# Kernel optimization log

Measured on AMD Instinct MI355X. Metric: run time of the kernel, lower is better.

## Reference

```python
import jax, jax.numpy as jnp
import numpy as np

B, S, H = 2, 256, 512
EPS = 1e-12  # TPLinker conditional LayerNorm default epsilon
NEG = -1e30  # finite stand-in for -inf in running max


def _cond_layer_norm(x, cond, Wg, Wb, gamma, beta):
    # TPLinker conditional LayerNorm: gamma/beta are modulated by a linear map of cond.
    g = gamma + cond @ Wg          # (..., H)
    b = beta + cond @ Wb           # (..., H)
    xc = x - jnp.mean(x, axis=-1, keepdims=True)
    inv = jax.lax.rsqrt(jnp.mean(xc * xc, axis=-1, keepdims=True) + EPS)
    return xc * inv * g + b


def setup_inputs() -> dict:
    key = jax.random.key(0)
    ks = jax.random.split(key, 6)
    return {
        "seq_hiddens": jax.random.normal(ks[0], (B, S, H), jnp.float32),
        "mask": jnp.ones((B, S), jnp.float32),
        "lamtha": jax.random.uniform(ks[1], (H,), jnp.float32),
        "Wg1": jax.random.normal(ks[2], (H, H), jnp.float32) * 0.02,
        "Wb1": jax.random.normal(ks[3], (H, H), jnp.float32) * 0.02,
        "g1": jnp.ones((H,), jnp.float32),
        "b1": jnp.zeros((H,), jnp.float32),
        "Wg2": jax.random.normal(ks[4], (H, H), jnp.float32) * 0.02,
        "Wb2": jax.random.normal(ks[5], (H, H), jnp.float32) * 0.02,
        "g2": jnp.ones((H,), jnp.float32),
        "b2": jnp.zeros((H,), jnp.float32),
    }


def reference(seq_hiddens, mask, lamtha, Wg1, Wb1, g1, b1, Wg2, Wb2, g2, b2):
    # mask additive penalty, broadcast over hidden (matches (1-mask)*-1000 expand)
    seq = seq_hiddens + ((1.0 - mask) * -1000.0)[:, :, None]  # (B,S,H)

    ii, jj = jnp.triu_indices(S)  # row-major pairs (i, j>=i), same order as the torch loop

    # window means over seq[i..j] via cumulative sums (replaces O(S^3) recomputation)
    csum = jnp.cumsum(seq, axis=1)                              # (B,S,H)
    lens = (jj - ii + 1).astype(seq.dtype)[None, :, None]
    mean_pairs = (csum[:, jj] - csum[:, ii] + seq[:, ii]) / lens  # (B,P,H)

    # window maxes over seq[i..j]: scan over j keeping running max per start i
    idx = jnp.arange(S)

    def step(state, j):
        sj = jnp.take(seq, j, axis=1)  # (B,H)
        new = jnp.where((idx <= j)[None, :, None],
                        jnp.maximum(state, sj[:, None, :]),
                        jnp.asarray(NEG, seq.dtype))
        return new, new

    _, Mall = jax.lax.scan(step, jnp.full((B, S, H), NEG, seq.dtype), idx)  # (S_j,B,S_i,H)
    max_pairs = Mall[jj, :, ii].transpose(1, 0, 2)  # (B,P,H)

    # mix pooling
    inner = lamtha * mean_pairs + (1.0 - lamtha) * max_pairs  # (B,P,H)

    visible = seq[:, jj]  # (B,P,H) token j
    repeat = seq[:, ii]   # (B,P,H) token i

    shaking = _cond_layer_norm(visible, repeat, Wg1, Wb1, g1, b1)
    return _cond_layer_norm(shaking, inner, Wg2, Wb2, g2, b2)
```

## Files before the change

kernel.cpp:

```cpp
#include <hip/hip_runtime.h>
#include <hip/hip_bf16.h>

typedef __hip_bfloat16 bf16;
typedef short short8 __attribute__((ext_vector_type(8)));
typedef float floatx4 __attribute__((ext_vector_type(4)));

#define S 256
#define H 512
#define P 32896
#define NROWS 65792
#define NEGF -1e30f
#define EPSF 1e-12f

#define OFF_SEQ    0u
#define OFF_CSUM   1048576u
#define OFF_LN1    2129920u
#define OFF_G1     3178496u
#define OFF_B1     4227072u
#define OFF_WCAT   5275648u
#define OFF_II     6324224u
#define OFF_JJ     6390016u
#define OFF_MU2    6455808u
#define OFF_INV2   6718976u
#define OFF_INNER  6982144u

__device__ __forceinline__ void gld_lds16(const void* g, void* l) {
    __builtin_amdgcn_global_load_lds(
        (const __attribute__((address_space(1))) void*)g,
        (__attribute__((address_space(3))) void*)l, 16, 0, 0);
}

__global__ __launch_bounds__(512) void prep_kernel(const float* __restrict__ Wg2,
                                                   const float* __restrict__ Wb2,
                                                   bf16* __restrict__ wcatT,
                                                   unsigned short* __restrict__ ii,
                                                   unsigned short* __restrict__ jj) {
    if (blockIdx.x < 1024) {
        int n = blockIdx.x, k = threadIdx.x;
        int tt = n >> 7, c = n & 127;
        int h = tt * 64 + (c & 63);
        float v = (c < 64) ? Wg2[(size_t)k * H + h] : Wb2[(size_t)k * H + h];
        wcatT[(size_t)n * H + k] = __float2bfloat16(v);
    } else {
        int p = (blockIdx.x - 1024) * 512 + threadIdx.x;
        if (p >= P) return;
        float disc = 513.0f * 513.0f - 8.0f * (float)p;
        int i = (int)((513.0f - sqrtf(disc)) * 0.5f);
        i = i < 0 ? 0 : (i > S - 1 ? S - 1 : i);
        while (i > 0 && (i * S - i * (i - 1) / 2) > p) --i;
        while (i < S - 1 && ((i + 1) * S - (i + 1) * i / 2) <= p) ++i;
        int off = i * S - i * (i - 1) / 2;
        ii[p] = (unsigned short)i;
        jj[p] = (unsigned short)(i + (p - off));
    }
}

__global__ __launch_bounds__(512) void seq_scan1_ln1(const float* __restrict__ x,
                                                     const float* __restrict__ mask,
                                                     float* __restrict__ seq, float* __restrict__ tot,
                                                     float* __restrict__ ln1) {
    __shared__ float part[8][8][2];
    __shared__ float rstat[8][2];
    int b = blockIdx.x >> 5, sc = blockIdx.x & 31, h = threadIdx.x;
    int wave = h >> 6, lane = h & 63;
    int s0 = sc * 8;
    float v[8];
    float run = 0.0f;
#pragma unroll
    for (int t = 0; t < 8; ++t) {
        int s = s0 + t;
        v[t] = x[(size_t)(b * S + s) * H + h] + (1.0f - mask[b * S + s]) * (-1000.0f);
        seq[(size_t)(b * S + s) * H + h] = v[t];
        run += v[t];
    }
    tot[(size_t)blockIdx.x * H + h] = run;
#pragma unroll
    for (int t = 0; t < 8; ++t) {
        float s = v[t], q = v[t] * v[t];
        for (int o = 1; o < 64; o <<= 1) { s += __shfl_xor(s, o); q += __shfl_xor(q, o); }
        if (lane == 0) { part[wave][t][0] = s; part[wave][t][1] = q; }
    }
    __syncthreads();
    if (h < 16) {
        int row = h >> 1, st = h & 1;
        float a = 0.0f;
#pragma unroll
        for (int w = 0; w < 8; ++w) a += part[w][row][st];
        rstat[row][st] = a;
    }
    __syncthreads();
#pragma unroll
    for (int t = 0; t < 8; ++t) {
        float m = rstat[t][0] * (1.0f / 512.0f);
        float var = rstat[t][1] * (1.0f / 512.0f) - m * m;
        var = var < 0.0f ? 0.0f : var;
        float inv = rsqrtf(var + EPSF);
        ln1[(size_t)(b * S + s0 + t) * H + h] = (v[t] - m) * inv;
    }
}

__global__ __launch_bounds__(512) void seq_scan2(const float* __restrict__ seq,
                                                 const float* __restrict__ tot,
                                                 float* __restrict__ csum) {
    int b = blockIdx.x >> 5, sc = blockIdx.x & 31, h = threadIdx.x;
    float run = 0.0f;
    for (int c = 0; c < sc; ++c) run += tot[(size_t)(b * 32 + c) * H + h];
    int s0 = sc * 8;
#pragma unroll
    for (int t = 0; t < 8; ++t) {
        run += seq[(size_t)(b * S + s0 + t) * H + h];
        csum[(size_t)(b * S + s0 + t) * H + h] = run;
    }
}

__global__ __launch_bounds__(512) void g1b1_kernel(
    const float* __restrict__ seq, const float* __restrict__ Wg1, const float* __restrict__ Wb1,
    const float* __restrict__ g1, const float* __restrict__ b1,
    float* __restrict__ G1, float* __restrict__ B1) {
    __shared__ float rowbuf[4][H];
    int grp = blockIdx.x;
    int mat = blockIdx.y;
    int h = threadIdx.x;
    int r0 = grp * 4;
    for (int r = 0; r < 4; ++r) rowbuf[r][h] = seq[(size_t)(r0 + r) * H + h];
    __syncthreads();
    const float* W = mat ? Wb1 : Wg1;
    float acc[4] = {0, 0, 0, 0};
#pragma unroll 8
    for (int k = 0; k < H; ++k) {
        float w = W[(size_t)k * H + h];
#pragma unroll
        for (int r = 0; r < 4; ++r) acc[r] += rowbuf[r][k] * w;
    }
    float bias = (mat ? b1 : g1)[h];
    float* dst = mat ? B1 : G1;
    for (int r = 0; r < 4; ++r) dst[(size_t)(r0 + r) * H + h] = acc[r] + bias;
}

__global__ __launch_bounds__(256) void inner_kernel(
    const float* __restrict__ seq, const float* __restrict__ csum,
    const float* __restrict__ lamtha, bf16* __restrict__ inner) {
    int id = blockIdx.x;
    int t = id & 255, b = id >> 8;
    int i = b ? (255 - t) : t;
    int h2 = threadIdx.x;
    float2 lam = ((const float2*)lamtha)[h2];
    float2 oml = {1.0f - lam.x, 1.0f - lam.y};
    const float2* seqb = (const float2*)(seq + (size_t)b * S * H);
    const float2* csb = (const float2*)(csum + (size_t)b * S * H);
    float2 s_i = seqb[i * 256 + h2];
    float2 c_i = csb[i * 256 + h2];
    float2 mrun = {NEGF, NEGF};
    size_t base = (size_t)b * P + (size_t)(i * S - i * (i - 1) / 2);
    __hip_bfloat162* dst = (__hip_bfloat162*)inner;
    int j = i;
#define INNER_STEP(vv, cc, jx)                                             \
    {                                                                      \
        mrun.x = fmaxf(mrun.x, vv.x);                                      \
        mrun.y = fmaxf(mrun.y, vv.y);                                      \
        float rl = 1.0f / (float)((jx) - i + 1);                           \
        float mx = (cc.x - c_i.x + s_i.x) * rl;                            \
        float my = (cc.y - c_i.y + s_i.y) * rl;                            \
        __hip_bfloat162 o;                                                 \
        o.x = __float2bfloat16(lam.x * mx + oml.x * mrun.x);               \
        o.y = __float2bfloat16(lam.y * my + oml.y * mrun.y);               \
        dst[(base + (size_t)((jx) - i)) * 256 + h2] = o;                   \
    }
    for (; j + 4 <= S; j += 4) {
        float2 v0 = seqb[(j + 0) * 256 + h2], c0 = csb[(j + 0) * 256 + h2];
        float2 v1 = seqb[(j + 1) * 256 + h2], c1 = csb[(j + 1) * 256 + h2];
        float2 v2 = seqb[(j + 2) * 256 + h2], c2 = csb[(j + 2) * 256 + h2];
        float2 v3 = seqb[(j + 3) * 256 + h2], c3 = csb[(j + 3) * 256 + h2];
        INNER_STEP(v0, c0, j + 0)
        INNER_STEP(v1, c1, j + 1)
        INNER_STEP(v2, c2, j + 2)
        INNER_STEP(v3, c3, j + 3)
    }
    for (; j < S; ++j) {
        float2 v = seqb[j * 256 + h2];
        float2 c = csb[j * 256 + h2];
        INNER_STEP(v, c, j)
    }
#undef INNER_STEP
}

__global__ void stats_kernel(const float* __restrict__ ln1, const float* __restrict__ G1,
                             const float* __restrict__ B1,
                             const unsigned short* __restrict__ ii,
                             const unsigned short* __restrict__ jj,
                             float* __restrict__ mu2, float* __restrict__ inv2) {
    int r = blockIdx.x * 4 + (threadIdx.x >> 6);
    int lane = threadIdx.x & 63;
    int b = (r >= P) ? 1 : 0;
    int p = r - b * P;
    int i = ii[p], j = jj[p];
    const float4* lp = (const float4*)(ln1 + (size_t)(b * S + j) * H);
    const float4* gp = (const float4*)(G1 + (size_t)(b * S + i) * H);
    const float4* bp = (const float4*)(B1 + (size_t)(b * S + i) * H);
    float sum = 0.0f, ss = 0.0f;
#pragma unroll
    for (int t = 0; t < 2; ++t) {
        int idx = t * 64 + lane;
        float4 a = lp[idx], g = gp[idx], bb = bp[idx];
        float v0 = a.x * g.x + bb.x, v1 = a.y * g.y + bb.y;
        float v2 = a.z * g.z + bb.z, v3 = a.w * g.w + bb.w;
        sum += (v0 + v1) + (v2 + v3);
        ss += (v0 * v0 + v1 * v1) + (v2 * v2 + v3 * v3);
    }
    for (int o = 1; o < 64; o <<= 1) { sum += __shfl_xor(sum, o); ss += __shfl_xor(ss, o); }
    if (lane == 0) {
        float m = sum * (1.0f / 512.0f);
        float var = ss * (1.0f / 512.0f) - m * m;
        var = var < 0.0f ? 0.0f : var;
        mu2[r] = m;
        inv2[r] = rsqrtf(var + EPSF);
    }
}

__global__ __launch_bounds__(256, 2) void gemm_kernel(
    const bf16* __restrict__ inner, const bf16* __restrict__ wcatT,
    const float* __restrict__ g2, const float* __restrict__ b2,
    const float* __restrict__ ln1, const float* __restrict__ G1, const float* __restrict__ B1,
    const unsigned short* __restrict__ ii, const unsigned short* __restrict__ jj,
    const float* __restrict__ mu2, const float* __restrict__ inv2,
    float* __restrict__ out) {
    extern __shared__ __align__(16) char smem[];

    const int tid = threadIdx.x;
    const int wave = tid >> 6, lane = tid & 63;
    const int q = lane >> 4, l15 = lane & 15;
    const int wm = wave & 1, wn = wave >> 1;

    const int id = blockIdx.x;
    int rb, t;
    if (id < 4096) { rb = (id >> 6) * 8 + (id & 7); t = (id >> 3) & 7; }
    else           { int w = id - 4096; rb = 512 + (w & 1); t = w >> 1; }
    const int R0 = rb * 128;

    const int srow = tid >> 3;
    const int sx8 = ((tid & 7) ^ (srow & 7)) * 8;
    const bf16* const Ag = inner + (size_t)(R0 + srow) * H + sx8;
    const bf16* const Bg = wcatT + (size_t)(t * 128 + srow) * H + sx8;

    char* const A0 = smem;
    char* const B0 = smem + 16384;
    char* const A1 = smem + 32768;
    char* const B1s = smem + 49152;

    floatx4 acc[4][4];
#pragma unroll
    for (int a = 0; a < 4; ++a)
#pragma unroll
        for (int c = 0; c < 4; ++c) acc[a][c] = (floatx4){0.f, 0.f, 0.f, 0.f};

    auto STAGE = [&](int kt, char* Ad, char* Bd) {
#pragma unroll
        for (int i2 = 0; i2 < 4; ++i2)
            gld_lds16(Ag + (size_t)i2 * 32 * H + kt * 64, Ad + i2 * 4096 + wave * 1024);
#pragma unroll
        for (int i2 = 0; i2 < 4; ++i2)
            gld_lds16(Bg + (size_t)i2 * 32 * H + kt * 64, Bd + i2 * 4096 + wave * 1024);
    };

    STAGE(0, A0, B0);
    STAGE(1, A1, B1s);
    asm volatile("s_waitcnt vmcnt(8)" ::: "memory");
    asm volatile("s_barrier" ::: "memory");

#pragma unroll
    for (int kt = 0; kt < 8; ++kt) {
        char* const As = (kt & 1) ? A1 : A0;
        char* const Bs = (kt & 1) ? B1s : B0;

        short8 bfr[4][2], af[4][2];
#pragma unroll
        for (int ks = 0; ks < 2; ++ks) {
#pragma unroll
            for (int fn = 0; fn < 4; ++fn) {
                int nr = (fn < 2 ? wn * 32 + fn * 16 : 64 + wn * 32 + (fn - 2) * 16) + l15;
                bfr[fn][ks] = *(const short8*)(Bs + nr * 128 + (((ks * 4 + q) ^ (l15 & 7)) << 4));
            }
#pragma unroll
            for (int fm = 0; fm < 4; ++fm) {
                int mr = wm * 64 + fm * 16 + l15;
                af[fm][ks] = *(const short8*)(As + mr * 128 + (((ks * 4 + q) ^ (l15 & 7)) << 4));
            }
        }

        __builtin_amdgcn_s_setprio(1);
#pragma unroll
        for (int fm = 0; fm < 4; ++fm)
#pragma unroll
            for (int fn = 0; fn < 4; ++fn)
                acc[fm][fn] = __builtin_amdgcn_mfma_f32_16x16x32_bf16(af[fm][0], bfr[fn][0], acc[fm][fn], 0, 0, 0);
        __builtin_amdgcn_s_setprio(0);

        if (kt < 6) {
            asm volatile("s_waitcnt lgkmcnt(0)" ::: "memory");
            asm volatile("s_barrier" ::: "memory");
            STAGE(kt + 2, As, Bs);
        }

        __builtin_amdgcn_s_setprio(1);
#pragma unroll
        for (int fm = 0; fm < 4; ++fm)
#pragma unroll
            for (int fn = 0; fn < 4; ++fn)
                acc[fm][fn] = __builtin_amdgcn_mfma_f32_16x16x32_bf16(af[fm][1], bfr[fn][1], acc[fm][fn], 0, 0, 0);
        __builtin_amdgcn_s_setprio(0);

        if (kt < 6) {
            asm volatile("s_waitcnt vmcnt(8)" ::: "memory");
            asm volatile("s_barrier" ::: "memory");
        } else if (kt == 6) {
            asm volatile("s_waitcnt vmcnt(0)" ::: "memory");
            asm volatile("s_barrier" ::: "memory");
        }
    }

    float g2v[2], b2v[2];
#pragma unroll
    for (int fg = 0; fg < 2; ++fg) {
        int h = t * 64 + wn * 32 + fg * 16 + l15;
        g2v[fg] = g2[h];
        b2v[fg] = b2[h];
    }
#pragma unroll
    for (int fm = 0; fm < 4; ++fm) {
#pragma unroll
        for (int r = 0; r < 4; ++r) {
            int m = wm * 64 + fm * 16 + q * 4 + r;
            int rg = R0 + m;
            int b = (rg >= P) ? 1 : 0;
            int p = rg - b * P;
            int i = ii[p], j = jj[p];
            float mu = mu2[rg], iv = inv2[rg];
            const float* lp = ln1 + (size_t)(b * S + j) * H + t * 64 + wn * 32;
            const float* gp = G1 + (size_t)(b * S + i) * H + t * 64 + wn * 32;
            const float* bp = B1 + (size_t)(b * S + i) * H + t * 64 + wn * 32;
            float* op = out + (size_t)rg * H + t * 64 + wn * 32;
#pragma unroll
            for (int fg = 0; fg < 2; ++fg) {
                int c = fg * 16 + l15;
                float s = (lp[c] * gp[c] + bp[c] - mu) * iv;
                float G2v = acc[fm][fg][r] + g2v[fg];
                float B2v = acc[fm][fg + 2][r] + b2v[fg];
                op[c] = s * G2v + B2v;
            }
        }
    }
}

extern "C" void kernel_launch(void* const* d_in, const int* in_sizes, int n_in,
                              void* d_out, int out_size, void* d_ws, size_t ws_size,
                              hipStream_t stream) {
    const float* x = (const float*)d_in[0];
    const float* mask = (const float*)d_in[1];
    const float* lamtha = (const float*)d_in[2];
    const float* Wg1 = (const float*)d_in[3];
    const float* Wb1 = (const float*)d_in[4];
    const float* g1 = (const float*)d_in[5];
    const float* b1 = (const float*)d_in[6];
    const float* Wg2 = (const float*)d_in[7];
    const float* Wb2 = (const float*)d_in[8];
    const float* g2 = (const float*)d_in[9];
    const float* b2 = (const float*)d_in[10];
    float* out = (float*)d_out;

    char* ws = (char*)d_ws;
    float* seq = (float*)(ws + OFF_SEQ);
    float* csum = (float*)(ws + OFF_CSUM);
    float* ln1 = (float*)(ws + OFF_LN1);
    float* G1 = (float*)(ws + OFF_G1);
    float* B1 = (float*)(ws + OFF_B1);
    bf16* wcatT = (bf16*)(ws + OFF_WCAT);
    unsigned short* iiA = (unsigned short*)(ws + OFF_II);
    unsigned short* jjA = (unsigned short*)(ws + OFF_JJ);
    float* mu2 = (float*)(ws + OFF_MU2);
    float* inv2 = (float*)(ws + OFF_INV2);
    bf16* inner = (bf16*)(ws + OFF_INNER);
    float* tot = (float*)(ws + OFF_INNER);

    static bool attr_set = false;
    if (!attr_set) {
        hipFuncSetAttribute((const void*)gemm_kernel,
                            hipFuncAttributeMaxDynamicSharedMemorySize, 65536);
        attr_set = true;
    }

    hipLaunchKernelGGL(prep_kernel, dim3(1089), dim3(512), 0, stream, Wg2, Wb2, wcatT, iiA, jjA);
    hipLaunchKernelGGL(seq_scan1_ln1, dim3(64), dim3(512), 0, stream, x, mask, seq, tot, ln1);
    hipLaunchKernelGGL(seq_scan2, dim3(64), dim3(512), 0, stream, seq, tot, csum);
    hipLaunchKernelGGL(g1b1_kernel, dim3(128, 2), dim3(512), 0, stream, seq, Wg1, Wb1, g1, b1, G1, B1);
    hipLaunchKernelGGL(inner_kernel, dim3(512), dim3(256), 0, stream, seq, csum, lamtha, inner);
    hipLaunchKernelGGL(stats_kernel, dim3(16448), dim3(256), 0, stream, ln1, G1, B1, iiA, jjA, mu2, inv2);
    hipLaunchKernelGGL(gemm_kernel, dim3(4112), dim3(256), 65536, stream,
                       inner, wcatT, g2, b2, ln1, G1, B1, iiA, jjA, mu2, inv2, out);
}
```

Baseline: 313.4 us.

## Fuse prep kernels and fold LN2 row stats into the inner pooling kernel

Merges the prep and first-scan kernels into one launch, and the second scan and G1/B1 matvec into another, cutting the launch count from seven to four. The per-pair LayerNorm-2 statistics are now computed inside the inner pooling kernel, which already walks every (i,j) pair, so the separate stats kernel that reread ln1/G1/B1 per pair goes away. The G1/B1 matvec also reads LDS rows as float4. In exchange the inner kernel does extra wave shuffles and LDS writes per j, which lengthens its serial loop, and there are only 512 blocks to carry that work.

```diff
diff --git a/kernel.cpp b/kernel.cpp
--- a/kernel.cpp
+++ b/kernel.cpp
@@ -30,131 +30,148 @@
         (__attribute__((address_space(3))) void*)l, 16, 0, 0);
 }
 
-__global__ __launch_bounds__(512) void prep_kernel(const float* __restrict__ Wg2,
-                                                   const float* __restrict__ Wb2,
-                                                   bf16* __restrict__ wcatT,
-                                                   unsigned short* __restrict__ ii,
-                                                   unsigned short* __restrict__ jj) {
-    if (blockIdx.x < 1024) {
-        int n = blockIdx.x, k = threadIdx.x;
-        int tt = n >> 7, c = n & 127;
-        int h = tt * 64 + (c & 63);
-        float v = (c < 64) ? Wg2[(size_t)k * H + h] : Wb2[(size_t)k * H + h];
-        wcatT[(size_t)n * H + k] = __float2bfloat16(v);
-    } else {
-        int p = (blockIdx.x - 1024) * 512 + threadIdx.x;
-        if (p >= P) return;
-        float disc = 513.0f * 513.0f - 8.0f * (float)p;
-        int i = (int)((513.0f - sqrtf(disc)) * 0.5f);
-        i = i < 0 ? 0 : (i > S - 1 ? S - 1 : i);
-        while (i > 0 && (i * S - i * (i - 1) / 2) > p) --i;
-        while (i < S - 1 && ((i + 1) * S - (i + 1) * i / 2) <= p) ++i;
-        int off = i * S - i * (i - 1) / 2;
-        ii[p] = (unsigned short)i;
-        jj[p] = (unsigned short)(i + (p - off));
-    }
-}
-
-__global__ __launch_bounds__(512) void seq_scan1_ln1(const float* __restrict__ x,
-                                                     const float* __restrict__ mask,
-                                                     float* __restrict__ seq, float* __restrict__ tot,
-                                                     float* __restrict__ ln1) {
+__global__ __launch_bounds__(512) void fusedA_kernel(
+    const float* __restrict__ x, const float* __restrict__ mask,
+    float* __restrict__ seq, float* __restrict__ tot, float* __restrict__ ln1,
+    const float* __restrict__ Wg2, const float* __restrict__ Wb2,
+    bf16* __restrict__ wcatT,
+    unsigned short* __restrict__ ii, unsigned short* __restrict__ jj) {
     __shared__ float part[8][8][2];
     __shared__ float rstat[8][2];
-    int b = blockIdx.x >> 5, sc = blockIdx.x & 31, h = threadIdx.x;
-    int wave = h >> 6, lane = h & 63;
-    int s0 = sc * 8;
-    float v[8];
-    float run = 0.0f;
-#pragma unroll
-    for (int t = 0; t < 8; ++t) {
-        int s = s0 + t;
-        v[t] = x[(size_t)(b * S + s) * H + h] + (1.0f - mask[b * S + s]) * (-1000.0f);
-        seq[(size_t)(b * S + s) * H + h] = v[t];
-        run += v[t];
-    }
-    tot[(size_t)blockIdx.x * H + h] = run;
-#pragma unroll
-    for (int t = 0; t < 8; ++t) {
-        float s = v[t], q = v[t] * v[t];
-        for (int o = 1; o < 64; o <<= 1) { s += __shfl_xor(s, o); q += __shfl_xor(q, o); }
-        if (lane == 0) { part[wave][t][0] = s; part[wave][t][1] = q; }
-    }
-    __syncthreads();
-    if (h < 16) {
-        int row = h >> 1, st = h & 1;
-        float a = 0.0f;
-#pragma unroll
-        for (int w = 0; w < 8; ++w) a += part[w][row][st];
-        rstat[row][st] = a;
-    }
-    __syncthreads();
-#pragma unroll
-    for (int t = 0; t < 8; ++t) {
-        float m = rstat[t][0] * (1.0f / 512.0f);
-        float var = rstat[t][1] * (1.0f / 512.0f) - m * m;
-        var = var < 0.0f ? 0.0f : var;
-        float inv = rsqrtf(var + EPSF);
-        ln1[(size_t)(b * S + s0 + t) * H + h] = (v[t] - m) * inv;
-    }
-}
-
-__global__ __launch_bounds__(512) void seq_scan2(const float* __restrict__ seq,
-                                                 const float* __restrict__ tot,
-                                                 float* __restrict__ csum) {
-    int b = blockIdx.x >> 5, sc = blockIdx.x & 31, h = threadIdx.x;
-    float run = 0.0f;
-    for (int c = 0; c < sc; ++c) run += tot[(size_t)(b * 32 + c) * H + h];
-    int s0 = sc * 8;
-#pragma unroll
-    for (int t = 0; t < 8; ++t) {
-        run += seq[(size_t)(b * S + s0 + t) * H + h];
-        csum[(size_t)(b * S + s0 + t) * H + h] = run;
-    }
-}
-
-__global__ __launch_bounds__(512) void g1b1_kernel(
-    const float* __restrict__ seq, const float* __restrict__ Wg1, const float* __restrict__ Wb1,
+    if (blockIdx.x < 64) {
+        int b = blockIdx.x >> 5, sc = blockIdx.x & 31, h = threadIdx.x;
+        int wave = h >> 6, lane = h & 63;
+        int s0 = sc * 8;
+        float v[8];
+        float run = 0.0f;
+#pragma unroll
+        for (int t = 0; t < 8; ++t) {
+            int s = s0 + t;
+            v[t] = x[(size_t)(b * S + s) * H + h] + (1.0f - mask[b * S + s]) * (-1000.0f);
+            seq[(size_t)(b * S + s) * H + h] = v[t];
+            run += v[t];
+        }
+        tot[(size_t)blockIdx.x * H + h] = run;
+#pragma unroll
+        for (int t = 0; t < 8; ++t) {
+            float s = v[t], q = v[t] * v[t];
+            for (int o = 1; o < 64; o <<= 1) { s += __shfl_xor(s, o); q += __shfl_xor(q, o); }
+            if (lane == 0) { part[wave][t][0] = s; part[wave][t][1] = q; }
+        }
+        __syncthreads();
+        if (h < 16) {
+            int row = h >> 1, st = h & 1;
+            float a = 0.0f;
+#pragma unroll
+            for (int w = 0; w < 8; ++w) a += part[w][row][st];
+            rstat[row][st] = a;
+        }
+        __syncthreads();
+#pragma unroll
+        for (int t = 0; t < 8; ++t) {
+            float m = rstat[t][0] * (1.0f / 512.0f);
+            float var = rstat[t][1] * (1.0f / 512.0f) - m * m;
+            var = var < 0.0f ? 0.0f : var;
+            float inv = rsqrtf(var + EPSF);
+            ln1[(size_t)(b * S + s0 + t) * H + h] = (v[t] - m) * inv;
+        }
+    } else {
+        int n = blockIdx.x - 64;
+        if (n < 1024) {
+            int k = threadIdx.x;
+            int tt = n >> 7, c = n & 127;
+            int h = tt * 64 + (c & 63);
+            float v = (c < 64) ? Wg2[(size_t)k * H + h] : Wb2[(size_t)k * H + h];
+            wcatT[(size_t)n * H + k] = __float2bfloat16(v);
+        } else {
+            int p = (n - 1024) * 512 + threadIdx.x;
+            if (p >= P) return;
+            float disc = 513.0f * 513.0f - 8.0f * (float)p;
+            int i = (int)((513.0f - sqrtf(disc)) * 0.5f);
+            i = i < 0 ? 0 : (i > S - 1 ? S - 1 : i);
+            while (i > 0 && (i * S - i * (i - 1) / 2) > p) --i;
+            while (i < S - 1 && ((i + 1) * S - (i + 1) * i / 2) <= p) ++i;
+            int off = i * S - i * (i - 1) / 2;
+            ii[p] = (unsigned short)i;
+            jj[p] = (unsigned short)(i + (p - off));
+        }
+    }
+}
+
+__global__ __launch_bounds__(512) void fusedB_kernel(
+    const float* __restrict__ seq, const float* __restrict__ tot,
+    float* __restrict__ csum,
+    const float* __restrict__ Wg1, const float* __restrict__ Wb1,
     const float* __restrict__ g1, const float* __restrict__ b1,
     float* __restrict__ G1, float* __restrict__ B1) {
     __shared__ float rowbuf[4][H];
-    int grp = blockIdx.x;
-    int mat = blockIdx.y;
-    int h = threadIdx.x;
-    int r0 = grp * 4;
-    for (int r = 0; r < 4; ++r) rowbuf[r][h] = seq[(size_t)(r0 + r) * H + h];
-    __syncthreads();
-    const float* W = mat ? Wb1 : Wg1;
-    float acc[4] = {0, 0, 0, 0};
-#pragma unroll 8
-    for (int k = 0; k < H; ++k) {
-        float w = W[(size_t)k * H + h];
-#pragma unroll
-        for (int r = 0; r < 4; ++r) acc[r] += rowbuf[r][k] * w;
-    }
-    float bias = (mat ? b1 : g1)[h];
-    float* dst = mat ? B1 : G1;
-    for (int r = 0; r < 4; ++r) dst[(size_t)(r0 + r) * H + h] = acc[r] + bias;
-}
-
-__global__ __launch_bounds__(256) void inner_kernel(
+    if (blockIdx.x < 64) {
+        int b = blockIdx.x >> 5, sc = blockIdx.x & 31, h = threadIdx.x;
+        float run = 0.0f;
+        for (int c = 0; c < sc; ++c) run += tot[(size_t)(b * 32 + c) * H + h];
+        int s0 = sc * 8;
+#pragma unroll
+        for (int t = 0; t < 8; ++t) {
+            run += seq[(size_t)(b * S + s0 + t) * H + h];
+            csum[(size_t)(b * S + s0 + t) * H + h] = run;
+        }
+    } else {
+        int idx = blockIdx.x - 64;
+        int grp = idx >> 1, mat = idx & 1;
+        int h = threadIdx.x;
+        int r0 = grp * 4;
+        for (int r = 0; r < 4; ++r) rowbuf[r][h] = seq[(size_t)(r0 + r) * H + h];
+        __syncthreads();
+        const float* W = mat ? Wb1 : Wg1;
+        float acc[4] = {0, 0, 0, 0};
+#pragma unroll 2
+        for (int k4 = 0; k4 < 128; ++k4) {
+            float4 r0v = ((const float4*)rowbuf[0])[k4];
+            float4 r1v = ((const float4*)rowbuf[1])[k4];
+            float4 r2v = ((const float4*)rowbuf[2])[k4];
+            float4 r3v = ((const float4*)rowbuf[3])[k4];
+            float w0 = W[(size_t)(k4 * 4 + 0) * H + h];
+            float w1 = W[(size_t)(k4 * 4 + 1) * H + h];
+            float w2 = W[(size_t)(k4 * 4 + 2) * H + h];
+            float w3 = W[(size_t)(k4 * 4 + 3) * H + h];
+            acc[0] += r0v.x * w0 + r0v.y * w1 + r0v.z * w2 + r0v.w * w3;
+            acc[1] += r1v.x * w0 + r1v.y * w1 + r1v.z * w2 + r1v.w * w3;
+            acc[2] += r2v.x * w0 + r2v.y * w1 + r2v.z * w2 + r2v.w * w3;
+            acc[3] += r3v.x * w0 + r3v.y * w1 + r3v.z * w2 + r3v.w * w3;
+        }
+        float bias = (mat ? b1 : g1)[h];
+        float* dst = mat ? B1 : G1;
+        for (int r = 0; r < 4; ++r) dst[(size_t)(r0 + r) * H + h] = acc[r] + bias;
+    }
+}
+
+__global__ __launch_bounds__(256) void inner_stats_kernel(
     const float* __restrict__ seq, const float* __restrict__ csum,
-    const float* __restrict__ lamtha, bf16* __restrict__ inner) {
+    const float* __restrict__ lamtha,
+    const float* __restrict__ ln1, const float* __restrict__ G1,
+    const float* __restrict__ B1,
+    bf16* __restrict__ inner, float* __restrict__ mu2, float* __restrict__ inv2) {
+    __shared__ float part[4][256][2];
     int id = blockIdx.x;
     int t = id & 255, b = id >> 8;
     int i = b ? (255 - t) : t;
     int h2 = threadIdx.x;
+    int wave = h2 >> 6, lane = h2 & 63;
     float2 lam = ((const float2*)lamtha)[h2];
     float2 oml = {1.0f - lam.x, 1.0f - lam.y};
     const float2* seqb = (const float2*)(seq + (size_t)b * S * H);
     const float2* csb = (const float2*)(csum + (size_t)b * S * H);
+    const float2* lnb = (const float2*)(ln1 + (size_t)b * S * H);
+    float2 gi = ((const float2*)(G1 + (size_t)(b * S + i) * H))[h2];
+    float2 bi = ((const float2*)(B1 + (size_t)(b * S + i) * H))[h2];
     float2 s_i = seqb[i * 256 + h2];
     float2 c_i = csb[i * 256 + h2];
     float2 mrun = {NEGF, NEGF};
-    size_t base = (size_t)b * P + (size_t)(i * S - i * (i - 1) / 2);
+    int pi = i * S - i * (i - 1) / 2;
+    size_t base = (size_t)b * P + (size_t)pi;
     __hip_bfloat162* dst = (__hip_bfloat162*)inner;
     int j = i;
-#define INNER_STEP(vv, cc, jx)                                             \
+#define INNER_STEP(vv, cc, aa, jx)                                         \
     {                                                                      \
         mrun.x = fmaxf(mrun.x, vv.x);                                      \
         mrun.y = fmaxf(mrun.y, vv.y);                                      \
@@ -165,53 +182,42 @@
         o.x = __float2bfloat16(lam.x * mx + oml.x * mrun.x);               \
         o.y = __float2bfloat16(lam.y * my + oml.y * mrun.y);               \
         dst[(base + (size_t)((jx) - i)) * 256 + h2] = o;                   \
+        float shx = aa.x * gi.x + bi.x;                                    \
+        float shy = aa.y * gi.y + bi.y;                                    \
+        float ps = shx + shy;                                              \
+        float pq = shx * shx + shy * shy;                                  \
+        for (int o2 = 1; o2 < 64; o2 <<= 1) {                              \
+            ps += __shfl_xor(ps, o2);                                      \
+            pq += __shfl_xor(pq, o2);                                      \
+        }                                                                  \
+        if (lane == 0) { part[wave][jx][0] = ps; part[wave][jx][1] = pq; } \
     }
     for (; j + 4 <= S; j += 4) {
-        float2 v0 = seqb[(j + 0) * 256 + h2], c0 = csb[(j + 0) * 256 + h2];
-        float2 v1 = seqb[(j + 1) * 256 + h2], c1 = csb[(j + 1) * 256 + h2];
-        float2 v2 = seqb[(j + 2) * 256 + h2], c2 = csb[(j + 2) * 256 + h2];
-        float2 v3 = seqb[(j + 3) * 256 + h2], c3 = csb[(j + 3) * 256 + h2];
-        INNER_STEP(v0, c0, j + 0)
-        INNER_STEP(v1, c1, j + 1)
-        INNER_STEP(v2, c2, j + 2)
-        INNER_STEP(v3, c3, j + 3)
+        float2 v0 = seqb[(j + 0) * 256 + h2], c0 = csb[(j + 0) * 256 + h2], a0 = lnb[(j + 0) * 256 + h2];
+        float2 v1 = seqb[(j + 1) * 256 + h2], c1 = csb[(j + 1) * 256 + h2], a1 = lnb[(j + 1) * 256 + h2];
+        float2 v2 = seqb[(j + 2) * 256 + h2], c2 = csb[(j + 2) * 256 + h2], a2 = lnb[(j + 2) * 256 + h2];
+        float2 v3 = seqb[(j + 3) * 256 + h2], c3 = csb[(j + 3) * 256 + h2], a3 = lnb[(j + 3) * 256 + h2];
+        INNER_STEP(v0, c0, a0, j + 0)
+        INNER_STEP(v1, c1, a1, j + 1)
+        INNER_STEP(v2, c2, a2, j + 2)
+        INNER_STEP(v3, c3, a3, j + 3)
     }
     for (; j < S; ++j) {
         float2 v = seqb[j * 256 + h2];
         float2 c = csb[j * 256 + h2];
-        INNER_STEP(v, c, j)
+        float2 a = lnb[j * 256 + h2];
+        INNER_STEP(v, c, a, j)
     }
 #undef INNER_STEP
-}
-
-__global__ void stats_kernel(const float* __restrict__ ln1, const float* __restrict__ G1,
-                             const float* __restrict__ B1,
-                             const unsigned short* __restrict__ ii,
-                             const unsigned short* __restrict__ jj,
-                             float* __restrict__ mu2, float* __restrict__ inv2) {
-    int r = blockIdx.x * 4 + (threadIdx.x >> 6);
-    int lane = threadIdx.x & 63;
-    int b = (r >= P) ? 1 : 0;
-    int p = r - b * P;
-    int i = ii[p], j = jj[p];
-    const float4* lp = (const float4*)(ln1 + (size_t)(b * S + j) * H);
-    const float4* gp = (const float4*)(G1 + (size_t)(b * S + i) * H);
-    const float4* bp = (const float4*)(B1 + (size_t)(b * S + i) * H);
-    float sum = 0.0f, ss = 0.0f;
-#pragma unroll
-    for (int t = 0; t < 2; ++t) {
-        int idx = t * 64 + lane;
-        float4 a = lp[idx], g = gp[idx], bb = bp[idx];
-        float v0 = a.x * g.x + bb.x, v1 = a.y * g.y + bb.y;
-        float v2 = a.z * g.z + bb.z, v3 = a.w * g.w + bb.w;
-        sum += (v0 + v1) + (v2 + v3);
-        ss += (v0 * v0 + v1 * v1) + (v2 * v2 + v3 * v3);
-    }
-    for (int o = 1; o < 64; o <<= 1) { sum += __shfl_xor(sum, o); ss += __shfl_xor(ss, o); }
-    if (lane == 0) {
+    __syncthreads();
+    int jo = h2;
+    if (jo >= i) {
+        float sum = part[0][jo][0] + part[1][jo][0] + part[2][jo][0] + part[3][jo][0];
+        float ssq = part[0][jo][1] + part[1][jo][1] + part[2][jo][1] + part[3][jo][1];
         float m = sum * (1.0f / 512.0f);
-        float var = ss * (1.0f / 512.0f) - m * m;
+        float var = ssq * (1.0f / 512.0f) - m * m;
         var = var < 0.0f ? 0.0f : var;
+        int r = b * P + pi + (jo - i);
         mu2[r] = m;
         inv2[r] = rsqrtf(var + EPSF);
     }
@@ -388,12 +394,12 @@
         attr_set = true;
     }
 
-    hipLaunchKernelGGL(prep_kernel, dim3(1089), dim3(512), 0, stream, Wg2, Wb2, wcatT, iiA, jjA);
-    hipLaunchKernelGGL(seq_scan1_ln1, dim3(64), dim3(512), 0, stream, x, mask, seq, tot, ln1);
-    hipLaunchKernelGGL(seq_scan2, dim3(64), dim3(512), 0, stream, seq, tot, csum);
-    hipLaunchKernelGGL(g1b1_kernel, dim3(128, 2), dim3(512), 0, stream, seq, Wg1, Wb1, g1, b1, G1, B1);
-    hipLaunchKernelGGL(inner_kernel, dim3(512), dim3(256), 0, stream, seq, csum, lamtha, inner);
-    hipLaunchKernelGGL(stats_kernel, dim3(16448), dim3(256), 0, stream, ln1, G1, B1, iiA, jjA, mu2, inv2);
+    hipLaunchKernelGGL(fusedA_kernel, dim3(1153), dim3(512), 0, stream,
+                       x, mask, seq, tot, ln1, Wg2, Wb2, wcatT, iiA, jjA);
+    hipLaunchKernelGGL(fusedB_kernel, dim3(320), dim3(512), 0, stream,
+                       seq, tot, csum, Wg1, Wb1, g1, b1, G1, B1);
+    hipLaunchKernelGGL(inner_stats_kernel, dim3(512), dim3(256), 0, stream,
+                       seq, csum, lamtha, ln1, G1, B1, inner, mu2, inv2);
     hipLaunchKernelGGL(gemm_kernel, dim3(4112), dim3(256), 65536, stream,
                        inner, wcatT, g2, b2, ln1, G1, B1, iiA, jjA, mu2, inv2, out);
 }
```

Measured after the change: 342.5 us. 9.3% more time.

## Enlarge GEMM tile to 256x256 with 512 threads and fuse prep kernels

Applied to the files above, without the earlier changes.

The main GEMM moves from 128x128 tiles with 256 threads to 256x256 tiles with 512 threads and a K-step of 32 over 16 iterations. The weight transpose layout and LDS swizzle are reworked to match. This raises data reuse per LDS load and cuts the block count. Separately, the small prep, scan and g1b1 kernels are merged into two launches to reduce launch overhead, and the g1b1 inner loop is vectorised over float4. The risks are higher register pressure (acc now holds 8x4 fragments) and fewer blocks per CU, which may hurt occupancy and latency hiding.

```diff
diff --git a/kernel.cpp b/kernel.cpp
--- a/kernel.cpp
+++ b/kernel.cpp
@@ -30,111 +30,120 @@
         (__attribute__((address_space(3))) void*)l, 16, 0, 0);
 }
 
-__global__ __launch_bounds__(512) void prep_kernel(const float* __restrict__ Wg2,
-                                                   const float* __restrict__ Wb2,
-                                                   bf16* __restrict__ wcatT,
-                                                   unsigned short* __restrict__ ii,
-                                                   unsigned short* __restrict__ jj) {
-    if (blockIdx.x < 1024) {
-        int n = blockIdx.x, k = threadIdx.x;
-        int tt = n >> 7, c = n & 127;
-        int h = tt * 64 + (c & 63);
-        float v = (c < 64) ? Wg2[(size_t)k * H + h] : Wb2[(size_t)k * H + h];
-        wcatT[(size_t)n * H + k] = __float2bfloat16(v);
-    } else {
-        int p = (blockIdx.x - 1024) * 512 + threadIdx.x;
-        if (p >= P) return;
-        float disc = 513.0f * 513.0f - 8.0f * (float)p;
-        int i = (int)((513.0f - sqrtf(disc)) * 0.5f);
-        i = i < 0 ? 0 : (i > S - 1 ? S - 1 : i);
-        while (i > 0 && (i * S - i * (i - 1) / 2) > p) --i;
-        while (i < S - 1 && ((i + 1) * S - (i + 1) * i / 2) <= p) ++i;
-        int off = i * S - i * (i - 1) / 2;
-        ii[p] = (unsigned short)i;
-        jj[p] = (unsigned short)(i + (p - off));
-    }
-}
-
-__global__ __launch_bounds__(512) void seq_scan1_ln1(const float* __restrict__ x,
-                                                     const float* __restrict__ mask,
-                                                     float* __restrict__ seq, float* __restrict__ tot,
-                                                     float* __restrict__ ln1) {
+__global__ __launch_bounds__(512) void fusedA_kernel(
+    const float* __restrict__ x, const float* __restrict__ mask,
+    float* __restrict__ seq, float* __restrict__ tot, float* __restrict__ ln1,
+    const float* __restrict__ Wg2, const float* __restrict__ Wb2,
+    bf16* __restrict__ wcatT,
+    unsigned short* __restrict__ ii, unsigned short* __restrict__ jj) {
     __shared__ float part[8][8][2];
     __shared__ float rstat[8][2];
-    int b = blockIdx.x >> 5, sc = blockIdx.x & 31, h = threadIdx.x;
-    int wave = h >> 6, lane = h & 63;
-    int s0 = sc * 8;
-    float v[8];
-    float run = 0.0f;
-#pragma unroll
-    for (int t = 0; t < 8; ++t) {
-        int s = s0 + t;
-        v[t] = x[(size_t)(b * S + s) * H + h] + (1.0f - mask[b * S + s]) * (-1000.0f);
-        seq[(size_t)(b * S + s) * H + h] = v[t];
-        run += v[t];
-    }
-    tot[(size_t)blockIdx.x * H + h] = run;
-#pragma unroll
-    for (int t = 0; t < 8; ++t) {
-        float s = v[t], q = v[t] * v[t];
-        for (int o = 1; o < 64; o <<= 1) { s += __shfl_xor(s, o); q += __shfl_xor(q, o); }
-        if (lane == 0) { part[wave][t][0] = s; part[wave][t][1] = q; }
-    }
-    __syncthreads();
-    if (h < 16) {
-        int row = h >> 1, st = h & 1;
-        float a = 0.0f;
-#pragma unroll
-        for (int w = 0; w < 8; ++w) a += part[w][row][st];
-        rstat[row][st] = a;
-    }
-    __syncthreads();
-#pragma unroll
-    for (int t = 0; t < 8; ++t) {
-        float m = rstat[t][0] * (1.0f / 512.0f);
-        float var = rstat[t][1] * (1.0f / 512.0f) - m * m;
-        var = var < 0.0f ? 0.0f : var;
-        float inv = rsqrtf(var + EPSF);
-        ln1[(size_t)(b * S + s0 + t) * H + h] = (v[t] - m) * inv;
-    }
-}
-
-__global__ __launch_bounds__(512) void seq_scan2(const float* __restrict__ seq,
-                                                 const float* __restrict__ tot,
-                                                 float* __restrict__ csum) {
-    int b = blockIdx.x >> 5, sc = blockIdx.x & 31, h = threadIdx.x;
-    float run = 0.0f;
-    for (int c = 0; c < sc; ++c) run += tot[(size_t)(b * 32 + c) * H + h];
-    int s0 = sc * 8;
-#pragma unroll
-    for (int t = 0; t < 8; ++t) {
-        run += seq[(size_t)(b * S + s0 + t) * H + h];
-        csum[(size_t)(b * S + s0 + t) * H + h] = run;
-    }
-}
-
-__global__ __launch_bounds__(512) void g1b1_kernel(
-    const float* __restrict__ seq, const float* __restrict__ Wg1, const float* __restrict__ Wb1,
+    if (blockIdx.x < 64) {
+        int b = blockIdx.x >> 5, sc = blockIdx.x & 31, h = threadIdx.x;
+        int wave = h >> 6, lane = h & 63;
+        int s0 = sc * 8;
+        float v[8];
+        float run = 0.0f;
+#pragma unroll
+        for (int t = 0; t < 8; ++t) {
+            int s = s0 + t;
+            v[t] = x[(size_t)(b * S + s) * H + h] + (1.0f - mask[b * S + s]) * (-1000.0f);
+            seq[(size_t)(b * S + s) * H + h] = v[t];
+            run += v[t];
+        }
+        tot[(size_t)blockIdx.x * H + h] = run;
+#pragma unroll
+        for (int t = 0; t < 8; ++t) {
+            float s = v[t], q = v[t] * v[t];
+            for (int o = 1; o < 64; o <<= 1) { s += __shfl_xor(s, o); q += __shfl_xor(q, o); }
+            if (lane == 0) { part[wave][t][0] = s; part[wave][t][1] = q; }
+        }
+        __syncthreads();
+        if (h < 16) {
+            int row = h >> 1, st = h & 1;
+            float a = 0.0f;
+#pragma unroll
+            for (int w = 0; w < 8; ++w) a += part[w][row][st];
+            rstat[row][st] = a;
+        }
+        __syncthreads();
+#pragma unroll
+        for (int t = 0; t < 8; ++t) {
+            float m = rstat[t][0] * (1.0f / 512.0f);
+            float var = rstat[t][1] * (1.0f / 512.0f) - m * m;
+            var = var < 0.0f ? 0.0f : var;
+            float inv = rsqrtf(var + EPSF);
+            ln1[(size_t)(b * S + s0 + t) * H + h] = (v[t] - m) * inv;
+        }
+    } else {
+        int n = blockIdx.x - 64;
+        if (n < 1024) {
+            int k = threadIdx.x;
+            int tt = n >> 8, c = n & 255;
+            int wn = c >> 6, u = c & 63;
+            int h = tt * 128 + wn * 32 + (u & 31);
+            float v = (u < 32) ? Wg2[(size_t)k * H + h] : Wb2[(size_t)k * H + h];
+            wcatT[(size_t)n * H + k] = __float2bfloat16(v);
+        } else {
+            int p = (n - 1024) * 512 + threadIdx.x;
+            if (p >= P) return;
+            float disc = 513.0f * 513.0f - 8.0f * (float)p;
+            int i = (int)((513.0f - sqrtf(disc)) * 0.5f);
+            i = i < 0 ? 0 : (i > S - 1 ? S - 1 : i);
+            while (i > 0 && (i * S - i * (i - 1) / 2) > p) --i;
+            while (i < S - 1 && ((i + 1) * S - (i + 1) * i / 2) <= p) ++i;
+            int off = i * S - i * (i - 1) / 2;
+            ii[p] = (unsigned short)i;
+            jj[p] = (unsigned short)(i + (p - off));
+        }
+    }
+}
+
+__global__ __launch_bounds__(512) void fusedB_kernel(
+    const float* __restrict__ seq, const float* __restrict__ tot,
+    float* __restrict__ csum,
+    const float* __restrict__ Wg1, const float* __restrict__ Wb1,
     const float* __restrict__ g1, const float* __restrict__ b1,
     float* __restrict__ G1, float* __restrict__ B1) {
     __shared__ float rowbuf[4][H];
-    int grp = blockIdx.x;
-    int mat = blockIdx.y;
-    int h = threadIdx.x;
-    int r0 = grp * 4;
-    for (int r = 0; r < 4; ++r) rowbuf[r][h] = seq[(size_t)(r0 + r) * H + h];
-    __syncthreads();
-    const float* W = mat ? Wb1 : Wg1;
-    float acc[4] = {0, 0, 0, 0};
-#pragma unroll 8
-    for (int k = 0; k < H; ++k) {
-        float w = W[(size_t)k * H + h];
-#pragma unroll
-        for (int r = 0; r < 4; ++r) acc[r] += rowbuf[r][k] * w;
-    }
-    float bias = (mat ? b1 : g1)[h];
-    float* dst = mat ? B1 : G1;
-    for (int r = 0; r < 4; ++r) dst[(size_t)(r0 + r) * H + h] = acc[r] + bias;
+    if (blockIdx.x < 64) {
+        int b = blockIdx.x >> 5, sc = blockIdx.x & 31, h = threadIdx.x;
+        float run = 0.0f;
+        for (int c = 0; c < sc; ++c) run += tot[(size_t)(b * 32 + c) * H + h];
+        int s0 = sc * 8;
+#pragma unroll
+        for (int t = 0; t < 8; ++t) {
+            run += seq[(size_t)(b * S + s0 + t) * H + h];
+            csum[(size_t)(b * S + s0 + t) * H + h] = run;
+        }
+    } else {
+        int idx = blockIdx.x - 64;
+        int grp = idx >> 1, mat = idx & 1;
+        int h = threadIdx.x;
+        int r0 = grp * 4;
+        for (int r = 0; r < 4; ++r) rowbuf[r][h] = seq[(size_t)(r0 + r) * H + h];
+        __syncthreads();
+        const float* W = mat ? Wb1 : Wg1;
+        float acc[4] = {0, 0, 0, 0};
+#pragma unroll 2
+        for (int k4 = 0; k4 < 128; ++k4) {
+            float4 r0v = ((const float4*)rowbuf[0])[k4];
+            float4 r1v = ((const float4*)rowbuf[1])[k4];
+            float4 r2v = ((const float4*)rowbuf[2])[k4];
+            float4 r3v = ((const float4*)rowbuf[3])[k4];
+            float w0 = W[(size_t)(k4 * 4 + 0) * H + h];
+            float w1 = W[(size_t)(k4 * 4 + 1) * H + h];
+            float w2 = W[(size_t)(k4 * 4 + 2) * H + h];
+            float w3 = W[(size_t)(k4 * 4 + 3) * H + h];
+            acc[0] += r0v.x * w0 + r0v.y * w1 + r0v.z * w2 + r0v.w * w3;
+            acc[1] += r1v.x * w0 + r1v.y * w1 + r1v.z * w2 + r1v.w * w3;
+            acc[2] += r2v.x * w0 + r2v.y * w1 + r2v.z * w2 + r2v.w * w3;
+            acc[3] += r3v.x * w0 + r3v.y * w1 + r3v.z * w2 + r3v.w * w3;
+        }
+        float bias = (mat ? b1 : g1)[h];
+        float* dst = mat ? B1 : G1;
+        for (int r = 0; r < 4; ++r) dst[(size_t)(r0 + r) * H + h] = acc[r] + bias;
+    }
 }
 
 __global__ __launch_bounds__(256) void inner_kernel(
@@ -217,7 +226,7 @@
     }
 }
 
-__global__ __launch_bounds__(256, 2) void gemm_kernel(
+__global__ __launch_bounds__(512, 4) void gemm_kernel(
     const bf16* __restrict__ inner, const bf16* __restrict__ wcatT,
     const float* __restrict__ g2, const float* __restrict__ b2,
     const float* __restrict__ ln1, const float* __restrict__ G1, const float* __restrict__ B1,
@@ -233,86 +242,88 @@
 
     const int id = blockIdx.x;
     int rb, t;
-    if (id < 4096) { rb = (id >> 6) * 8 + (id & 7); t = (id >> 3) & 7; }
-    else           { int w = id - 4096; rb = 512 + (w & 1); t = w >> 1; }
-    const int R0 = rb * 128;
-
-    const int srow = tid >> 3;
-    const int sx8 = ((tid & 7) ^ (srow & 7)) * 8;
-    const bf16* const Ag = inner + (size_t)(R0 + srow) * H + sx8;
-    const bf16* const Bg = wcatT + (size_t)(t * 128 + srow) * H + sx8;
-
-    char* const A0 = smem;
-    char* const B0 = smem + 16384;
-    char* const A1 = smem + 32768;
-    char* const B1s = smem + 49152;
-
-    floatx4 acc[4][4];
-#pragma unroll
-    for (int a = 0; a < 4; ++a)
+    if (id < 1024) { rb = (id >> 5) * 8 + (id & 7); t = (id >> 3) & 3; }
+    else           { rb = 256; t = id - 1024; }
+    const int R0 = rb * 256;
+
+    int row0, cq0, row1, cq1;
+    {
+        int ci = tid;
+        int pr = ci >> 3, pc = ci & 7, l = pc ^ (pr & 7);
+        row0 = (pr << 1) | (l >> 2); cq0 = l & 3;
+    }
+    {
+        int ci = 512 + tid;
+        int pr = ci >> 3, pc = ci & 7, l = pc ^ (pr & 7);
+        row1 = (pr << 1) | (l >> 2); cq1 = l & 3;
+    }
+    const bf16* const Ag0 = inner + (size_t)(R0 + row0) * H + cq0 * 8;
+    const bf16* const Ag1 = inner + (size_t)(R0 + row1) * H + cq1 * 8;
+    const bf16* const Bg0 = wcatT + (size_t)(t * 256 + row0) * H + cq0 * 8;
+    const bf16* const Bg1 = wcatT + (size_t)(t * 256 + row1) * H + cq1 * 8;
+
+    const int prl = l15 >> 1;
+    const int apc = (((((l15 & 1) << 2) | q)) ^ prl) << 4;
+    const int C = prl * 128 + apc;
+
+    floatx4 acc[8][4];
+#pragma unroll
+    for (int a = 0; a < 8; ++a)
 #pragma unroll
         for (int c = 0; c < 4; ++c) acc[a][c] = (floatx4){0.f, 0.f, 0.f, 0.f};
 
-    auto STAGE = [&](int kt, char* Ad, char* Bd) {
-#pragma unroll
-        for (int i2 = 0; i2 < 4; ++i2)
-            gld_lds16(Ag + (size_t)i2 * 32 * H + kt * 64, Ad + i2 * 4096 + wave * 1024);
-#pragma unroll
-        for (int i2 = 0; i2 < 4; ++i2)
-            gld_lds16(Bg + (size_t)i2 * 32 * H + kt * 64, Bd + i2 * 4096 + wave * 1024);
+    auto STAGE = [&](int kt, int bufbase) {
+        gld_lds16(Ag0 + kt * 32, smem + bufbase + wave * 1024);
+        gld_lds16(Ag1 + kt * 32, smem + bufbase + 8192 + wave * 1024);
+        gld_lds16(Bg0 + kt * 32, smem + bufbase + 16384 + wave * 1024);
+        gld_lds16(Bg1 + kt * 32, smem + bufbase + 24576 + wave * 1024);
     };
 
-    STAGE(0, A0, B0);
-    STAGE(1, A1, B1s);
-    asm volatile("s_waitcnt vmcnt(8)" ::: "memory");
+    STAGE(0, 0);
+    STAGE(1, 32768);
+    asm volatile("s_waitcnt vmcnt(4)" ::: "memory");
     asm volatile("s_barrier" ::: "memory");
 
 #pragma unroll
-    for (int kt = 0; kt < 8; ++kt) {
-        char* const As = (kt & 1) ? A1 : A0;
-        char* const Bs = (kt & 1) ? B1s : B0;
-
-        short8 bfr[4][2], af[4][2];
-#pragma unroll
-        for (int ks = 0; ks < 2; ++ks) {
-#pragma unroll
-            for (int fn = 0; fn < 4; ++fn) {
-                int nr = (fn < 2 ? wn * 32 + fn * 16 : 64 + wn * 32 + (fn - 2) * 16) + l15;
-                bfr[fn][ks] = *(const short8*)(Bs + nr * 128 + (((ks * 4 + q) ^ (l15 & 7)) << 4));
-            }
-#pragma unroll
-            for (int fm = 0; fm < 4; ++fm) {
-                int mr = wm * 64 + fm * 16 + l15;
-                af[fm][ks] = *(const short8*)(As + mr * 128 + (((ks * 4 + q) ^ (l15 & 7)) << 4));
-            }
-        }
+    for (int kt = 0; kt < 16; ++kt) {
+        const int bufbase = (kt & 1) ? 32768 : 0;
+        const char* As = smem + bufbase;
+        const char* Bs = As + 16384;
+
+        short8 af[8], bfr[4];
+#pragma unroll
+        for (int fn = 0; fn < 4; ++fn)
+            bfr[fn] = *(const short8*)(Bs + wn * 4096 + fn * 1024 + C);
+#pragma unroll
+        for (int fm = 0; fm < 8; ++fm)
+            af[fm] = *(const short8*)(As + wm * 8192 + fm * 1024 + C);
 
         __builtin_amdgcn_s_setprio(1);
 #pragma unroll
         for (int fm = 0; fm < 4; ++fm)
 #pragma unroll
             for (int fn = 0; fn < 4; ++fn)
-                acc[fm][fn] = __builtin_amdgcn_mfma_f32_16x16x32_bf16(af[fm][0], bfr[fn][0], acc[fm][fn], 0, 0, 0);
+                acc[fm][fn] = __builtin_amdgcn_mfma_f32_16x16x32_bf16(af[fm], bfr[fn], acc[fm][fn], 0, 0, 0);
         __builtin_amdgcn_s_setprio(0);
 
-        if (kt < 6) {
+        if (kt < 14) {
             asm volatile("s_waitcnt lgkmcnt(0)" ::: "memory");
             asm volatile("s_barrier" ::: "memory");
-            STAGE(kt + 2, As, Bs);
+            STAGE(kt + 2, bufbase);
         }
 
         __builtin_amdgcn_s_setprio(1);
 #pragma unroll
-        for (int fm = 0; fm < 4; ++fm)
+        for (int fm = 4; fm < 8; ++fm)
 #pragma unroll
             for (int fn = 0; fn < 4; ++fn)
-                acc[fm][fn] = __builtin_amdgcn_mfma_f32_16x16x32_bf16(af[fm][1], bfr[fn][1], acc[fm][fn], 0, 0, 0);
+                acc[fm][fn] = __builtin_amdgcn_mfma_f32_16x16x32_bf16(af[fm], bfr[fn], acc[fm][fn], 0, 0, 0);
         __builtin_amdgcn_s_setprio(0);
 
-        if (kt < 6) {
-            asm volatile("s_waitcnt vmcnt(8)" ::: "memory");
+        if (kt < 14) {
+            asm volatile("s_waitcnt vmcnt(4)" ::: "memory");
             asm volatile("s_barrier" ::: "memory");
-        } else if (kt == 6) {
+        } else if (kt == 14) {
             asm volatile("s_waitcnt vmcnt(0)" ::: "memory");
             asm volatile("s_barrier" ::: "memory");
         }
@@ -321,24 +332,24 @@
     float g2v[2], b2v[2];
 #pragma unroll
     for (int fg = 0; fg < 2; ++fg) {
-        int h = t * 64 + wn * 32 + fg * 16 + l15;
+        int h = t * 128 + wn * 32 + fg * 16 + l15;
         g2v[fg] = g2[h];
         b2v[fg] = b2[h];
     }
 #pragma unroll
-    for (int fm = 0; fm < 4; ++fm) {
+    for (int fm = 0; fm < 8; ++fm) {
 #pragma unroll
         for (int r = 0; r < 4; ++r) {
-            int m = wm * 64 + fm * 16 + q * 4 + r;
+            int m = wm * 128 + fm * 16 + q * 4 + r;
             int rg = R0 + m;
             int b = (rg >= P) ? 1 : 0;
             int p = rg - b * P;
             int i = ii[p], j = jj[p];
             float mu = mu2[rg], iv = inv2[rg];
-            const float* lp = ln1 + (size_t)(b * S + j) * H + t * 64 + wn * 32;
-            const float* gp = G1 + (size_t)(b * S + i) * H + t * 64 + wn * 32;
-            const float* bp = B1 + (size_t)(b * S + i) * H + t * 64 + wn * 32;
-            float* op = out + (size_t)rg * H + t * 64 + wn * 32;
+            const float* lp = ln1 + (size_t)(b * S + j) * H + t * 128 + wn * 32;
+            const float* gp = G1 + (size_t)(b * S + i) * H + t * 128 + wn * 32;
+            const float* bp = B1 + (size_t)(b * S + i) * H + t * 128 + wn * 32;
+            float* op = out + (size_t)rg * H + t * 128 + wn * 32;
 #pragma unroll
             for (int fg = 0; fg < 2; ++fg) {
                 int c = fg * 16 + l15;
@@ -388,12 +399,14 @@
         attr_set = true;
     }
 
-    hipLaunchKernelGGL(prep_kernel, dim3(1089), dim3(512), 0, stream, Wg2, Wb2, wcatT, iiA, jjA);
-    hipLaunchKernelGGL(seq_scan1_ln1, dim3(64), dim3(512), 0, stream, x, mask, seq, tot, ln1);
-    hipLaunchKernelGGL(seq_scan2, dim3(64), dim3(512), 0, stream, seq, tot, csum);
-    hipLaunchKernelGGL(g1b1_kernel, dim3(128, 2), dim3(512), 0, stream, seq, Wg1, Wb1, g1, b1, G1, B1);
-    hipLaunchKernelGGL(inner_kernel, dim3(512), dim3(256), 0, stream, seq, csum, lamtha, inner);
-    hipLaunchKernelGGL(stats_kernel, dim3(16448), dim3(256), 0, stream, ln1, G1, B1, iiA, jjA, mu2, inv2);
-    hipLaunchKernelGGL(gemm_kernel, dim3(4112), dim3(256), 65536, stream,
+    hipLaunchKernelGGL(fusedA_kernel, dim3(1153), dim3(512), 0, stream,
+                       x, mask, seq, tot, ln1, Wg2, Wb2, wcatT, iiA, jjA);
+    hipLaunchKernelGGL(fusedB_kernel, dim3(320), dim3(512), 0, stream,
+                       seq, tot, csum, Wg1, Wb1, g1, b1, G1, B1);
+    hipLaunchKernelGGL(inner_kernel, dim3(512), dim3(256), 0, stream,
+                       seq, csum, lamtha, inner);
+    hipLaunchKernelGGL(stats_kernel, dim3(16448), dim3(256), 0, stream,
+                       ln1, G1, B1, iiA, jjA, mu2, inv2);
+    hipLaunchKernelGGL(gemm_kernel, dim3(1028), dim3(512), 65536, stream,
                        inner, wcatT, g2, b2, ln1, G1, B1, iiA, jjA, mu2, inv2, out);
 }
```

Measured after the change: 1.023 ms. 3.26x slower.
